# Kernel tuning notes

Measured on AMD Instinct MI355X. Metric: run time of the kernel, lower is better.

The kernel has to match this reference:

```python
import jax, jax.numpy as jnp
import numpy as np

BN_EPS = 1e-5


def setup_inputs() -> dict:
    key = jax.random.key(0)
    ks = jax.random.split(key, 6)
    N, C, T, V, S = 64, 64, 300, 25, 3
    x = jax.random.normal(ks[0], (N, C, T, V), dtype=jnp.float32)
    A = jax.random.uniform(ks[1], (S, V, V), dtype=jnp.float32)
    PA1 = jnp.ones((S, V, V), dtype=jnp.float32)
    PA2 = jax.random.normal(ks[2], (S, V, V), dtype=jnp.float32) * 1e-3
    Wc = jax.random.normal(ks[3], (S, C, C), dtype=jnp.float32) * np.sqrt(2.0 / (C * S))
    bc = jnp.zeros((S, C), dtype=jnp.float32)
    gamma = jnp.ones((C,), dtype=jnp.float32)
    beta = jnp.zeros((C,), dtype=jnp.float32)
    rmean = jnp.zeros((C,), dtype=jnp.float32)
    rvar = jnp.ones((C,), dtype=jnp.float32)
    return {"x": x, "A": A, "PA1": PA1, "PA2": PA2, "Wc": Wc, "bc": bc,
            "gamma": gamma, "beta": beta, "rmean": rmean, "rvar": rvar}


def reference(x, A, PA1, PA2, Wc, bc, gamma, beta, rmean, rvar):
    # x: (N, C, T, V); A/PA1/PA2: (S, V, V); Wc: (S, out_c, in_c); bc: (S, out_c)
    Ae = A * PA1 + PA2  # adaptive adjacency, (S, V, V)
    S = Ae.shape[0]
    y = None
    for i in range(S):  # small fixed loop over graph subsets
        # graph aggregation over joints: (N,C,T,V) @ (V,V) -> (N,C,T,V)
        xa = jnp.einsum('nctv,vw->nctw', x, Ae[i])
        # 1x1 conv over channels + bias
        z = jnp.einsum('nctw,oc->notw', xa, Wc[i]) + bc[i][None, :, None, None]
        y = z if y is None else y + z
    # BatchNorm2d (inference form with running stats)
    scale = gamma / jnp.sqrt(rvar + BN_EPS)
    y = y * scale[None, :, None, None] + (beta - rmean * scale)[None, :, None, None]
    # residual: in_channels == out_channels -> down is identity
    y = y + x
    return jax.nn.relu(y)
```

## Files before the change

### kernel.cpp

```cpp
#include <hip/hip_runtime.h>

typedef _Float16 half_t;
typedef __attribute__((ext_vector_type(8))) _Float16 half8;
typedef __attribute__((ext_vector_type(4))) _Float16 half4;
typedef __attribute__((ext_vector_type(4))) float float4_t;

#define BN_EPS 1e-5f

constexpr int Nn = 64, Cc = 64, Tt = 300, Vv = 25, Ss = 3;
constexpr int XA_S = 72;

__global__ __launch_bounds__(256, 1)
void gcn_pre(const float* __restrict__ A,   const float* __restrict__ PA1,
             const float* __restrict__ PA2, const float* __restrict__ Wc,
             const float* __restrict__ bc,  const float* __restrict__ gamma,
             const float* __restrict__ beta, const float* __restrict__ rmean,
             const float* __restrict__ rvar,
             half_t* __restrict__ aeh, half_t* __restrict__ wch,
             float* __restrict__ bnsc, float* __restrict__ bnsh)
{
    const int tid = threadIdx.x;
    if (tid < Cc) {
        float sc   = gamma[tid] * rsqrtf(rvar[tid] + BN_EPS);
        float bsum = bc[tid] + bc[Cc + tid] + bc[2 * Cc + tid];
        bnsc[tid] = sc;
        bnsh[tid] = beta[tid] - rmean[tid] * sc + bsum * sc;
    }
    for (int e = tid; e < Ss * 2 * 64; e += 256) {
        int s = e >> 7, wt = (e >> 6) & 1, lane = e & 63;
        int col = lane & 15, q = lane >> 4;
        int w = wt * 16 + col;
        #pragma unroll
        for (int j = 0; j < 8; ++j) {
            int v = q * 8 + j;
            float val = 0.f;
            if (v < Vv && w < Vv) {
                int ai = (s * Vv + v) * Vv + w;
                val = A[ai] * PA1[ai] + PA2[ai];
            }
            aeh[e * 8 + j] = (half_t)val;
        }
    }
    for (int e = tid; e < Ss * 4 * 2 * 64; e += 256) {
        int s = e >> 9, r = e & 511, ot = r >> 7, ks = (r >> 6) & 1, lane = r & 63;
        int col = lane & 15, q = lane >> 4;
        int o = ot * 16 + col;
        #pragma unroll
        for (int j = 0; j < 8; ++j) {
            int c = ks * 32 + q * 8 + j;
            wch[e * 8 + j] = (half_t)Wc[(s * Cc + o) * Cc + c];
        }
    }
}

__global__ __launch_bounds__(256, 3)
void gcn_fused(const float* __restrict__ x, const half_t* __restrict__ aeh,
               const half_t* __restrict__ wch, const float* __restrict__ bnsc,
               const float* __restrict__ bnsh, float* __restrict__ out)
{
    __shared__ __align__(16) float xs[Cc * 100];
    __shared__ __align__(16) half_t xaW[4][32][XA_S];

    const int tid  = threadIdx.x;
    const int lane = tid & 63;
    const int wave = tid >> 6;
    const int col  = lane & 15;
    const int quad = lane >> 4;

    const int n  = blockIdx.y;
    const int t0 = blockIdx.x * 4;
    const float* xb = x + (size_t)n * Cc * Tt * Vv + t0 * Vv;

    for (int i = tid; i < 1600; i += 256) {
        int c = i / 25, q = i - c * 25;
        const float* g = xb + c * (Tt * Vv) + q * 4;
        __builtin_amdgcn_global_load_lds(
            (const __attribute__((address_space(1))) unsigned int*)g,
            (__attribute__((address_space(3))) unsigned int*)&xs[i * 4],
            16, 0, 0);
    }

    half8 ab[Ss][2];
    #pragma unroll
    for (int s = 0; s < Ss; ++s)
        #pragma unroll
        for (int wt = 0; wt < 2; ++wt)
            ab[s][wt] = *(const half8*)&aeh[((s * 2 + wt) * 64 + lane) * 8];

    __syncthreads();

    half8 af[4];
    #pragma unroll
    for (int ct = 0; ct < 4; ++ct) {
        const float* r = &xs[(ct * 16 + col) * 100 + wave * 25];
        half8 h;
        if (quad < 3) {
            #pragma unroll
            for (int j = 0; j < 8; ++j) h[j] = (half_t)r[quad * 8 + j];
        } else {
            h[0] = (half_t)r[24];
            #pragma unroll
            for (int j = 1; j < 8; ++j) h[j] = (half_t)0.f;
        }
        af[ct] = h;
    }

    const float4_t zero4 = {0.f, 0.f, 0.f, 0.f};
    float4_t yacc[4][2];
    #pragma unroll
    for (int ot = 0; ot < 4; ++ot)
        #pragma unroll
        for (int wt = 0; wt < 2; ++wt) yacc[ot][wt] = zero4;

    #pragma unroll
    for (int s = 0; s < Ss; ++s) {
        #pragma unroll
        for (int ct = 0; ct < 4; ++ct)
            #pragma unroll
            for (int wt = 0; wt < 2; ++wt) {
                float4_t r = __builtin_amdgcn_mfma_f32_16x16x32_f16(af[ct], ab[s][wt], zero4, 0, 0, 0);
                half4 h;
                #pragma unroll
                for (int i = 0; i < 4; ++i) h[i] = (half_t)r[i];
                *(half4*)&xaW[wave][wt * 16 + col][ct * 16 + quad * 4] = h;
            }
        half8 bf[2][2];
        #pragma unroll
        for (int ks = 0; ks < 2; ++ks)
            #pragma unroll
            for (int wt = 0; wt < 2; ++wt)
                bf[ks][wt] = *(const half8*)&xaW[wave][wt * 16 + col][ks * 32 + quad * 8];
        #pragma unroll
        for (int ot = 0; ot < 4; ++ot) {
            half8 w0 = *(const half8*)&wch[(((s * 4 + ot) * 2 + 0) * 64 + lane) * 8];
            half8 w1 = *(const half8*)&wch[(((s * 4 + ot) * 2 + 1) * 64 + lane) * 8];
            #pragma unroll
            for (int wt = 0; wt < 2; ++wt) {
                yacc[ot][wt] = __builtin_amdgcn_mfma_f32_16x16x32_f16(w0, bf[0][wt], yacc[ot][wt], 0, 0, 0);
                yacc[ot][wt] = __builtin_amdgcn_mfma_f32_16x16x32_f16(w1, bf[1][wt], yacc[ot][wt], 0, 0, 0);
            }
        }
    }

    #pragma unroll
    for (int ot = 0; ot < 4; ++ot) {
        float4_t sc = *(const float4_t*)&bnsc[ot * 16 + quad * 4];
        float4_t sh = *(const float4_t*)&bnsh[ot * 16 + quad * 4];
        #pragma unroll
        for (int i = 0; i < 4; ++i) {
            const int o = ot * 16 + quad * 4 + i;
            #pragma unroll
            for (int wt = 0; wt < 2; ++wt) {
                int w = wt * 16 + col;
                if (w < Vv) {
                    const int idx = o * 100 + wave * 25 + w;
                    float val = yacc[ot][wt][i] * sc[i] + sh[i] + xs[idx];
                    xs[idx] = fmaxf(val, 0.f);
                }
            }
        }
    }

    __syncthreads();

    float* ob = out + (size_t)n * Cc * Tt * Vv + t0 * Vv;
    for (int i = tid; i < 1600; i += 256) {
        int c = i / 25, q = i - c * 25;
        *(float4_t*)(ob + c * (Tt * Vv) + q * 4) = *(const float4_t*)&xs[i * 4];
    }
}

extern "C" void kernel_launch(void* const* d_in, const int* in_sizes, int n_in,
                              void* d_out, int out_size, void* d_ws, size_t ws_size,
                              hipStream_t stream) {
    const float* x     = (const float*)d_in[0];
    const float* A     = (const float*)d_in[1];
    const float* PA1   = (const float*)d_in[2];
    const float* PA2   = (const float*)d_in[3];
    const float* Wc    = (const float*)d_in[4];
    const float* bc    = (const float*)d_in[5];
    const float* gamma = (const float*)d_in[6];
    const float* beta  = (const float*)d_in[7];
    const float* rmean = (const float*)d_in[8];
    const float* rvar  = (const float*)d_in[9];
    float* out = (float*)d_out;

    half_t* aeh = (half_t*)d_ws;
    half_t* wch = aeh + Ss * 2 * 64 * 8;
    float* bnsc = (float*)(wch + Ss * 4 * 2 * 64 * 8);
    float* bnsh = bnsc + Cc;

    gcn_pre<<<dim3(1), 256, 0, stream>>>(A, PA1, PA2, Wc, bc, gamma, beta, rmean, rvar,
                                         aeh, wch, bnsc, bnsh);
    gcn_fused<<<dim3(Tt / 4, Nn), 256, 0, stream>>>(x, aeh, wch, bnsc, bnsh, out);
}
```

Baseline: 286.4 us.

## Process eight time steps per block with fp16 padded LDS tile

Each block now covers 8 time steps instead of 4, and each wave loops over two time steps. This spreads the per-block setup cost (adjacency fragment loads, launch overhead) over more work and halves the grid size. The input tile is converted to fp16 on load and stored in a padded [c][t][32] LDS layout, so MFMA A-fragments become single vector reads instead of gathered scalar conversions. The asynchronous global-to-LDS copy becomes register loads with scattered half stores. The residual and final output now pass through fp16, which adds rounding error to the result, and the fewer, larger blocks may lower occupancy.

After: 305.2 us. 6.6% more time.

```diff
diff --git a/kernel.cpp b/kernel.cpp
--- a/kernel.cpp
+++ b/kernel.cpp
@@ -9,6 +9,8 @@
 
 constexpr int Nn = 64, Cc = 64, Tt = 300, Vv = 25, Ss = 3;
 constexpr int XA_S = 72;
+constexpr int TB   = 8;
+constexpr int XH_S = 264;
 
 __global__ __launch_bounds__(256, 1)
 void gcn_pre(const float* __restrict__ A,   const float* __restrict__ PA1,
@@ -58,7 +60,7 @@
                const half_t* __restrict__ wch, const float* __restrict__ bnsc,
                const float* __restrict__ bnsh, float* __restrict__ out)
 {
-    __shared__ __align__(16) float xs[Cc * 100];
+    __shared__ __align__(16) half_t xh[Cc * XH_S];
     __shared__ __align__(16) half_t xaW[4][32][XA_S];
 
     const int tid  = threadIdx.x;
@@ -68,16 +70,31 @@
     const int quad = lane >> 4;
 
     const int n  = blockIdx.y;
-    const int t0 = blockIdx.x * 4;
+    const int t0 = blockIdx.x * TB;
+    const int tlim = min(TB, Tt - t0);
+    const int nq   = (tlim * Vv) / 4;
     const float* xb = x + (size_t)n * Cc * Tt * Vv + t0 * Vv;
 
-    for (int i = tid; i < 1600; i += 256) {
-        int c = i / 25, q = i - c * 25;
-        const float* g = xb + c * (Tt * Vv) + q * 4;
-        __builtin_amdgcn_global_load_lds(
-            (const __attribute__((address_space(1))) unsigned int*)g,
-            (__attribute__((address_space(3))) unsigned int*)&xs[i * 4],
-            16, 0, 0);
+    for (int i = tid; i < Cc * TB * 7; i += 256) {
+        int c = i / 56, r = i - c * 56, t = r / 7, v = 25 + r - (r / 7) * 7;
+        xh[c * XH_S + t * 32 + v] = (half_t)0.f;
+    }
+
+    #pragma unroll
+    for (int k = 0; k < 13; ++k) {
+        int f = tid + k * 256;
+        if (f < Cc * 50) {
+            int c = f / 50, q = f - c * 50;
+            if (q < nq) {
+                float4_t d = *(const float4_t*)(xb + c * (Tt * Vv) + q * 4);
+                int g = q * 4;
+                #pragma unroll
+                for (int j = 0; j < 4; ++j) {
+                    int gg = g + j, t = gg / 25, v = gg - t * 25;
+                    xh[c * XH_S + t * 32 + v] = (half_t)d[j];
+                }
+            }
+        }
     }
 
     half8 ab[Ss][2];
@@ -89,84 +106,93 @@
 
     __syncthreads();
 
-    half8 af[4];
+    const float4_t zero4 = {0.f, 0.f, 0.f, 0.f};
+
+    for (int tt = 0; tt < 2; ++tt) {
+        const int tl = tt * 4 + wave;
+        const int tg = t0 + tl;
+        if (tg < Tt) {
+            half8 af[4];
+            #pragma unroll
+            for (int ct = 0; ct < 4; ++ct)
+                af[ct] = *(const half8*)&xh[(ct * 16 + col) * XH_S + tl * 32 + quad * 8];
+
+            float4_t yacc[4][2];
+            #pragma unroll
+            for (int ot = 0; ot < 4; ++ot)
+                #pragma unroll
+                for (int wt = 0; wt < 2; ++wt) yacc[ot][wt] = zero4;
+
+            #pragma unroll
+            for (int s = 0; s < Ss; ++s) {
+                #pragma unroll
+                for (int ct = 0; ct < 4; ++ct)
+                    #pragma unroll
+                    for (int wt = 0; wt < 2; ++wt) {
+                        float4_t r = __builtin_amdgcn_mfma_f32_16x16x32_f16(af[ct], ab[s][wt], zero4, 0, 0, 0);
+                        half4 h;
+                        #pragma unroll
+                        for (int i = 0; i < 4; ++i) h[i] = (half_t)r[i];
+                        *(half4*)&xaW[wave][wt * 16 + col][ct * 16 + quad * 4] = h;
+                    }
+                half8 bf[2][2];
+                #pragma unroll
+                for (int ks = 0; ks < 2; ++ks)
+                    #pragma unroll
+                    for (int wt = 0; wt < 2; ++wt)
+                        bf[ks][wt] = *(const half8*)&xaW[wave][wt * 16 + col][ks * 32 + quad * 8];
+                #pragma unroll
+                for (int ot = 0; ot < 4; ++ot) {
+                    half8 w0 = *(const half8*)&wch[(((s * 4 + ot) * 2 + 0) * 64 + lane) * 8];
+                    half8 w1 = *(const half8*)&wch[(((s * 4 + ot) * 2 + 1) * 64 + lane) * 8];
+                    #pragma unroll
+                    for (int wt = 0; wt < 2; ++wt) {
+                        yacc[ot][wt] = __builtin_amdgcn_mfma_f32_16x16x32_f16(w0, bf[0][wt], yacc[ot][wt], 0, 0, 0);
+                        yacc[ot][wt] = __builtin_amdgcn_mfma_f32_16x16x32_f16(w1, bf[1][wt], yacc[ot][wt], 0, 0, 0);
+                    }
+                }
+            }
+
+            #pragma unroll
+            for (int ot = 0; ot < 4; ++ot) {
+                float4_t sc = *(const float4_t*)&bnsc[ot * 16 + quad * 4];
+                float4_t sh = *(const float4_t*)&bnsh[ot * 16 + quad * 4];
+                #pragma unroll
+                for (int i = 0; i < 4; ++i) {
+                    const int o = ot * 16 + quad * 4 + i;
+                    #pragma unroll
+                    for (int wt = 0; wt < 2; ++wt) {
+                        int w = wt * 16 + col;
+                        if (w < Vv) {
+                            const int idx = o * XH_S + tl * 32 + w;
+                            float val = yacc[ot][wt][i] * sc[i] + sh[i] + (float)xh[idx];
+                            xh[idx] = (half_t)fmaxf(val, 0.f);
+                        }
+                    }
+                }
+            }
+        }
+    }
+
+    __syncthreads();
+
+    float* ob = out + (size_t)n * Cc * Tt * Vv + t0 * Vv;
     #pragma unroll
-    for (int ct = 0; ct < 4; ++ct) {
-        const float* r = &xs[(ct * 16 + col) * 100 + wave * 25];
-        half8 h;
-        if (quad < 3) {
-            #pragma unroll
-            for (int j = 0; j < 8; ++j) h[j] = (half_t)r[quad * 8 + j];
-        } else {
-            h[0] = (half_t)r[24];
-            #pragma unroll
-            for (int j = 1; j < 8; ++j) h[j] = (half_t)0.f;
-        }
-        af[ct] = h;
-    }
-
-    const float4_t zero4 = {0.f, 0.f, 0.f, 0.f};
-    float4_t yacc[4][2];
-    #pragma unroll
-    for (int ot = 0; ot < 4; ++ot)
-        #pragma unroll
-        for (int wt = 0; wt < 2; ++wt) yacc[ot][wt] = zero4;
-
-    #pragma unroll
-    for (int s = 0; s < Ss; ++s) {
-        #pragma unroll
-        for (int ct = 0; ct < 4; ++ct)
-            #pragma unroll
-            for (int wt = 0; wt < 2; ++wt) {
-                float4_t r = __builtin_amdgcn_mfma_f32_16x16x32_f16(af[ct], ab[s][wt], zero4, 0, 0, 0);
-                half4 h;
-                #pragma unroll
-                for (int i = 0; i < 4; ++i) h[i] = (half_t)r[i];
-                *(half4*)&xaW[wave][wt * 16 + col][ct * 16 + quad * 4] = h;
-            }
-        half8 bf[2][2];
-        #pragma unroll
-        for (int ks = 0; ks < 2; ++ks)
-            #pragma unroll
-            for (int wt = 0; wt < 2; ++wt)
-                bf[ks][wt] = *(const half8*)&xaW[wave][wt * 16 + col][ks * 32 + quad * 8];
-        #pragma unroll
-        for (int ot = 0; ot < 4; ++ot) {
-            half8 w0 = *(const half8*)&wch[(((s * 4 + ot) * 2 + 0) * 64 + lane) * 8];
-            half8 w1 = *(const half8*)&wch[(((s * 4 + ot) * 2 + 1) * 64 + lane) * 8];
-            #pragma unroll
-            for (int wt = 0; wt < 2; ++wt) {
-                yacc[ot][wt] = __builtin_amdgcn_mfma_f32_16x16x32_f16(w0, bf[0][wt], yacc[ot][wt], 0, 0, 0);
-                yacc[ot][wt] = __builtin_amdgcn_mfma_f32_16x16x32_f16(w1, bf[1][wt], yacc[ot][wt], 0, 0, 0);
-            }
-        }
-    }
-
-    #pragma unroll
-    for (int ot = 0; ot < 4; ++ot) {
-        float4_t sc = *(const float4_t*)&bnsc[ot * 16 + quad * 4];
-        float4_t sh = *(const float4_t*)&bnsh[ot * 16 + quad * 4];
-        #pragma unroll
-        for (int i = 0; i < 4; ++i) {
-            const int o = ot * 16 + quad * 4 + i;
-            #pragma unroll
-            for (int wt = 0; wt < 2; ++wt) {
-                int w = wt * 16 + col;
-                if (w < Vv) {
-                    const int idx = o * 100 + wave * 25 + w;
-                    float val = yacc[ot][wt][i] * sc[i] + sh[i] + xs[idx];
-                    xs[idx] = fmaxf(val, 0.f);
-                }
-            }
-        }
-    }
-
-    __syncthreads();
-
-    float* ob = out + (size_t)n * Cc * Tt * Vv + t0 * Vv;
-    for (int i = tid; i < 1600; i += 256) {
-        int c = i / 25, q = i - c * 25;
-        *(float4_t*)(ob + c * (Tt * Vv) + q * 4) = *(const float4_t*)&xs[i * 4];
+    for (int k = 0; k < 13; ++k) {
+        int f = tid + k * 256;
+        if (f < Cc * 50) {
+            int c = f / 50, q = f - c * 50;
+            if (q < nq) {
+                int g = q * 4;
+                float4_t d;
+                #pragma unroll
+                for (int j = 0; j < 4; ++j) {
+                    int gg = g + j, t = gg / 25, v = gg - t * 25;
+                    d[j] = (float)xh[c * XH_S + t * 32 + v];
+                }
+                *(float4_t*)(ob + c * (Tt * Vv) + q * 4) = d;
+            }
+        }
     }
 }
 
@@ -192,5 +218,5 @@
 
     gcn_pre<<<dim3(1), 256, 0, stream>>>(A, PA1, PA2, Wc, bc, gamma, beta, rmean, rvar,
                                          aeh, wch, bnsc, bnsh);
-    gcn_fused<<<dim3(Tt / 4, Nn), 256, 0, stream>>>(x, aeh, wch, bnsc, bnsh, out);
+    gcn_fused<<<dim3((Tt + TB - 1) / TB, Nn), 256, 0, stream>>>(x, aeh, wch, bnsc, bnsh, out);
 }
```
